# Performance work log

Hardware: AMD Instinct MI355X
Metric: run time of the kernel (lower is better)

## Reference

```python
import jax, jax.numpy as jnp
import numpy as np

D_MODEL = 1024
NUM_HEADS = 16
D_K = D_MODEL // NUM_HEADS


def setup_inputs() -> dict:
    key = jax.random.key(0)
    k1, k2, k3, k4 = jax.random.split(key, 4)
    x = jax.random.normal(k1, (2, 2048, D_MODEL), dtype=jnp.float32)
    # qkv_proj: Linear(d_model, 3*d_model, bias=False); stored as [in, out] for x @ W
    W_qkv = jax.random.normal(k2, (D_MODEL, 3 * D_MODEL), dtype=jnp.float32) * (1.0 / np.sqrt(D_MODEL))
    W_out = jax.random.normal(k3, (D_MODEL, D_MODEL), dtype=jnp.float32) * (1.0 / np.sqrt(D_MODEL))
    b_out = jax.random.normal(k4, (D_MODEL,), dtype=jnp.float32) * 0.01
    return {"x": x, "W_qkv": W_qkv, "W_out": W_out, "b_out": b_out}


def reference(x, W_qkv, W_out, b_out):
    B, N, C = x.shape
    scale = 1.0 / np.sqrt(D_K)
    qkv = (x @ W_qkv).reshape(B, N, 3, NUM_HEADS, D_K)
    qkv = jnp.transpose(qkv, (2, 0, 3, 1, 4))  # [3, B, H, N, d_k]
    q, k, v = qkv[0], qkv[1], qkv[2]
    scores = jnp.einsum("bhqd,bhkd->bhqk", q, k) * scale  # [B,H,N,N]
    attn = jax.nn.softmax(scores, axis=-1)
    out = jnp.einsum("bhqk,bhkd->bhqd", attn, v)  # [B,H,N,d_k]
    out = jnp.transpose(out, (0, 2, 1, 3)).reshape(B, N, C)
    return out @ W_out + b_out
```

## Files before the change

### kernel.cpp

```cpp
#include <hip/hip_runtime.h>
#include <cstdint>

typedef __bf16 bf16_t;
typedef __bf16 bf16x4 __attribute__((ext_vector_type(4)));
typedef __bf16 bf16x8 __attribute__((ext_vector_type(8)));
typedef float  f32x4  __attribute__((ext_vector_type(4)));
typedef uint32_t u32x4 __attribute__((ext_vector_type(4)));

#define MFMA16(a,b,c) __builtin_amdgcn_mfma_f32_16x16x32_bf16((a),(b),(c),0,0,0)
#define BAR()    __builtin_amdgcn_s_barrier()
#define VMW(n)   asm volatile("s_waitcnt vmcnt(" #n ")" ::: "memory")

__device__ __forceinline__ void gload_lds16(const bf16_t* g, bf16_t* l) {
  __builtin_amdgcn_global_load_lds(
      (const __attribute__((address_space(1))) unsigned int*)g,
      (__attribute__((address_space(3))) unsigned int*)l,
      16, 0, 0);
}

__device__ __forceinline__ uint32_t cvt_pk_bf16(float lo, float hi) {
  uint32_t r;
  asm("v_cvt_pk_bf16_f32 %0, %1, %2" : "=v"(r) : "v"(lo), "v"(hi));
  return r;
}

__global__ void k_conv_x(const float* __restrict__ x, bf16_t* __restrict__ xb) {
  int i = blockIdx.x * blockDim.x + threadIdx.x;
  const float4* p = reinterpret_cast<const float4*>(x) + (size_t)i * 2;
  float4 a = p[0], b = p[1];
  bf16x8 v;
  v[0]=(bf16_t)a.x; v[1]=(bf16_t)a.y; v[2]=(bf16_t)a.z; v[3]=(bf16_t)a.w;
  v[4]=(bf16_t)b.x; v[5]=(bf16_t)b.y; v[6]=(bf16_t)b.z; v[7]=(bf16_t)b.w;
  *reinterpret_cast<bf16x8*>(xb + (size_t)i * 8) = v;
}

__global__ void k_transpose_w2(const float* __restrict__ Wq, bf16_t* __restrict__ WqT,
                               const float* __restrict__ Wo, bf16_t* __restrict__ WoT) {
  __shared__ float tile[32][33];
  int bx = blockIdx.x;
  const float* W; bf16_t* WT; int N, n0;
  if (bx < 96) { W = Wq; WT = WqT; N = 3072; n0 = bx * 32; }
  else         { W = Wo; WT = WoT; N = 1024; n0 = (bx - 96) * 32; }
  int k0 = blockIdx.y * 32;
  int c = threadIdx.x & 31, r8 = threadIdx.x >> 5;
#pragma unroll
  for (int rr = 0; rr < 4; rr++) {
    int r = r8 + rr * 8;
    tile[r][c] = W[(size_t)(k0 + r) * N + n0 + c];
  }
  __syncthreads();
#pragma unroll
  for (int rr = 0; rr < 4; rr++) {
    int r = r8 + rr * 8;
    WT[(size_t)(n0 + r) * 1024 + k0 + c] = (bf16_t)tile[c][r];
  }
}

template<int EPI, int MT, int NT>
__global__ __launch_bounds__(256, 2) void k_gemm(
    const bf16_t* __restrict__ A, const bf16_t* __restrict__ BT, int Klen,
    bf16_t* __restrict__ Qo, bf16_t* __restrict__ Ko, bf16_t* __restrict__ Vt,
    const float* __restrict__ bias, float* __restrict__ Out, int Nout) {
  constexpr int WM = MT / 2;
  constexpr int MF = WM / 16;
  constexpr int WN = NT / 2;
  constexpr int NF = WN / 16;
  __shared__ bf16_t As[2][MT * 32];
  __shared__ bf16_t Bs[2][NT * 32];
  int tid = threadIdx.x, lane = tid & 63, wid = tid >> 6;
  int row0 = blockIdx.x * MT, col0 = blockIdx.y * NT;
  int wr = wid >> 1, wc = wid & 1;
  int g = lane >> 4, li = lane & 15;

  f32x4 acc[MF][NF] = {};

  auto stage = [&](int buf, int kt) {
    int k0 = kt * 32;
#pragma unroll
    for (int j = 0; j < MT / 64; j++) {
      int q = tid + 256 * j;
      int r = q >> 2, part = q & 3;
      gload_lds16(A + (size_t)(row0 + r) * Klen + k0 + part * 8,
                  &As[buf][q * 8]);
    }
#pragma unroll
    for (int j = 0; j < NT / 64; j++) {
      int q = tid + 256 * j;
      int r = q >> 2, part = q & 3;
      gload_lds16(BT + (size_t)(col0 + r) * Klen + k0 + part * 8,
                  &Bs[buf][q * 8]);
    }
  };

  int nk = Klen >> 5;
  stage(0, 0);
  for (int kt = 0; kt < nk; kt++) {
    __syncthreads();
    if (kt + 1 < nk) stage((kt + 1) & 1, kt + 1);
    int buf = kt & 1;
    int kl = g * 8;
    bf16x8 a[MF], b[NF];
#pragma unroll
    for (int m = 0; m < MF; m++)
      a[m] = *reinterpret_cast<const bf16x8*>(&As[buf][(wr * WM + m * 16 + li) * 32 + kl]);
#pragma unroll
    for (int n = 0; n < NF; n++)
      b[n] = *reinterpret_cast<const bf16x8*>(&Bs[buf][(wc * WN + n * 16 + li) * 32 + kl]);
#pragma unroll
    for (int m = 0; m < MF; m++)
#pragma unroll
      for (int n = 0; n < NF; n++)
        acc[m][n] = MFMA16(a[m], b[n], acc[m][n]);
  }

#pragma unroll
  for (int m = 0; m < MF; m++) {
    int rg = row0 + wr * WM + m * 16 + g * 4;
    int b2 = rg >> 11, nn0 = rg & 2047;
#pragma unroll
    for (int n = 0; n < NF; n++) {
      int cg = col0 + wc * WN + n * 16 + li;
      if constexpr (EPI == 0) {
        int t = cg >> 10, h = (cg >> 6) & 15, dk = cg & 63;
        int head = (b2 << 4) + h;
        if (t == 2) {
          bf16x4 pv;
#pragma unroll
          for (int ii = 0; ii < 4; ii++) pv[ii] = (bf16_t)acc[m][n][ii];
          *reinterpret_cast<bf16x4*>(
              &Vt[(size_t)head * 131072 + (size_t)dk * 2048 + nn0]) = pv;
        } else {
#pragma unroll
          for (int ii = 0; ii < 4; ii++) {
            float v = acc[m][n][ii];
            size_t idx = ((size_t)head * 2048 + nn0 + ii) * 64 + dk;
            if (t == 0) Qo[idx] = (bf16_t)(v * 0.18033688011112042f);
            else        Ko[idx] = (bf16_t)v;
          }
        }
      } else {
#pragma unroll
        for (int ii = 0; ii < 4; ii++)
          Out[(size_t)(rg + ii) * Nout + cg] = acc[m][n][ii] + bias[cg];
      }
    }
  }
}

__global__ __launch_bounds__(256, 2) void k_flash(
    const bf16_t* __restrict__ Q, const bf16_t* __restrict__ K,
    const bf16_t* __restrict__ VT, bf16_t* __restrict__ O) {
  __shared__ bf16_t Ks[3][64 * 64];
  __shared__ bf16_t Vs[3][64 * 64];

  int bi = (blockIdx.x & 7) * 64 + (blockIdx.x >> 3);
  int head = bi >> 4, qt = bi & 15;
  int tid = threadIdx.x, lane = tid & 63, wid = tid >> 6;
  int g = lane >> 4, li = lane & 15;

  const bf16_t* Qh = Q + (size_t)head * 131072 + (size_t)qt * 128 * 64;
  const bf16_t* Kh = K + (size_t)head * 131072;
  const bf16_t* Vh = VT + (size_t)head * 131072;

  bf16x8 qf[2][2];
#pragma unroll
  for (int rg = 0; rg < 2; rg++) {
    const bf16_t* qrow = Qh + (size_t)(wid * 32 + rg * 16 + li) * 64;
    qf[rg][0] = *reinterpret_cast<const bf16x8*>(qrow + g * 8);
    qf[rg][1] = *reinterpret_cast<const bf16x8*>(qrow + 32 + g * 8);
  }

  u32x4 onesw;
  onesw[0] = 0x3F803F80u; onesw[1] = 0x3F803F80u;
  onesw[2] = 0x3F803F80u; onesw[3] = 0x3F803F80u;
  bf16x8 ones = __builtin_bit_cast(bf16x8, onesw);

  f32x4 zero4 = {};
  f32x4 o[2][4] = {};
  f32x4 osum[2] = {};

  auto stage = [&](int buf, int t) {
    int kv0 = t * 64;
#pragma unroll
    for (int j = 0; j < 2; j++) {
      int q = tid + 256 * j;
      int key = q >> 3, part = q & 7;
      int sw = (key & 7) ^ (((key >> 3) & 3) << 1);
      gload_lds16(Kh + (size_t)(kv0 + key) * 64 + ((part ^ sw) * 8),
                  &Ks[buf][(tid + j * 256) * 8]);
    }
#pragma unroll
    for (int j = 0; j < 2; j++) {
      int q = tid + 256 * j;
      int dv = q >> 3, part = q & 7;
      gload_lds16(Vh + (size_t)dv * 2048 + kv0 + ((part ^ (dv & 7)) * 8),
                  &Vs[buf][(tid + j * 256) * 8]);
    }
  };

  stage(0, 0);
  stage(1, 1);
  for (int t = 0; t < 32; t++) {
    if (t < 31) { VMW(4); } else { VMW(0); }
    BAR();
    __builtin_amdgcn_sched_barrier(0);
    if (t + 2 < 32) stage((t + 2) % 3, t + 2);
    int buf = t % 3;
    char* KsB = (char*)&Ks[buf][0];
    char* VsB = (char*)&Vs[buf][0];

    bf16x8 ka[2][4];
#pragma unroll
    for (int kd = 0; kd < 2; kd++)
#pragma unroll
      for (int nf = 0; nf < 4; nf++) {
        int key = ((li >> 2) << 3) | ((nf & 1) << 2) | (li & 3) | ((nf >> 1) << 5);
        int sw = (key & 7) ^ (((key >> 3) & 3) << 1);
        ka[kd][nf] = *reinterpret_cast<const bf16x8*>(
            KsB + key * 128 + (((kd * 4 + g) ^ sw) << 4));
      }

    f32x4 s[2][4];
    __builtin_amdgcn_s_setprio(1);
#pragma unroll
    for (int nf = 0; nf < 4; nf++) {
      s[0][nf] = MFMA16(ka[0][nf], qf[0][0], zero4);
      s[1][nf] = MFMA16(ka[0][nf], qf[1][0], zero4);
    }
#pragma unroll
    for (int nf = 0; nf < 4; nf++) {
      s[0][nf] = MFMA16(ka[1][nf], qf[0][1], s[0][nf]);
      s[1][nf] = MFMA16(ka[1][nf], qf[1][1], s[1][nf]);
    }
    __builtin_amdgcn_s_setprio(0);

    bf16x8 pa[2][2];
#pragma unroll
    for (int rg = 0; rg < 2; rg++) {
#pragma unroll
      for (int nf = 0; nf < 4; nf++)
#pragma unroll
        for (int i = 0; i < 4; i++)
          s[rg][nf][i] = __builtin_amdgcn_exp2f(s[rg][nf][i]);
      u32x4 w0, w1;
      w0[0] = cvt_pk_bf16(s[rg][0][0], s[rg][0][1]);
      w0[1] = cvt_pk_bf16(s[rg][0][2], s[rg][0][3]);
      w0[2] = cvt_pk_bf16(s[rg][1][0], s[rg][1][1]);
      w0[3] = cvt_pk_bf16(s[rg][1][2], s[rg][1][3]);
      w1[0] = cvt_pk_bf16(s[rg][2][0], s[rg][2][1]);
      w1[1] = cvt_pk_bf16(s[rg][2][2], s[rg][2][3]);
      w1[2] = cvt_pk_bf16(s[rg][3][0], s[rg][3][1]);
      w1[3] = cvt_pk_bf16(s[rg][3][2], s[rg][3][3]);
      pa[rg][0] = __builtin_bit_cast(bf16x8, w0);
      pa[rg][1] = __builtin_bit_cast(bf16x8, w1);
    }

    __builtin_amdgcn_s_setprio(1);
    osum[0] = MFMA16(pa[0][0], ones, osum[0]);
    osum[0] = MFMA16(pa[0][1], ones, osum[0]);
    osum[1] = MFMA16(pa[1][0], ones, osum[1]);
    osum[1] = MFMA16(pa[1][1], ones, osum[1]);
#pragma unroll
    for (int nfv = 0; nfv < 4; nfv++) {
      int dv = nfv * 16 + li;
      bf16x8 b0 = *reinterpret_cast<const bf16x8*>(
          VsB + dv * 128 + ((g * 16) ^ ((dv & 7) << 4)));
      bf16x8 b1 = *reinterpret_cast<const bf16x8*>(
          VsB + dv * 128 + ((64 + g * 16) ^ ((dv & 7) << 4)));
      o[0][nfv] = MFMA16(pa[0][0], b0, o[0][nfv]);
      o[0][nfv] = MFMA16(pa[0][1], b1, o[0][nfv]);
      o[1][nfv] = MFMA16(pa[1][0], b0, o[1][nfv]);
      o[1][nfv] = MFMA16(pa[1][1], b1, o[1][nfv]);
    }
    __builtin_amdgcn_s_setprio(0);
  }

  int b2 = head >> 4, h = head & 15;
#pragma unroll
  for (int rg = 0; rg < 2; rg++) {
#pragma unroll
    for (int i = 0; i < 4; i++) {
      float inv = 1.f / osum[rg][i];
      int n = qt * 128 + wid * 32 + rg * 16 + g * 4 + i;
      size_t base = ((size_t)b2 * 2048 + n) * 1024 + h * 64;
#pragma unroll
      for (int nfv = 0; nfv < 4; nfv++)
        O[base + nfv * 16 + li] = (bf16_t)(o[rg][nfv][i] * inv);
    }
  }
}

extern "C" void kernel_launch(void* const* d_in, const int* in_sizes, int n_in,
                              void* d_out, int out_size, void* d_ws, size_t ws_size,
                              hipStream_t stream) {
  const float* x    = (const float*)d_in[0];
  const float* Wqkv = (const float*)d_in[1];
  const float* Wout = (const float*)d_in[2];
  const float* bout = (const float*)d_in[3];
  float* out = (float*)d_out;

  char* ws = (char*)d_ws;
  bf16_t* xb    = (bf16_t*)(ws);
  bf16_t* wqkvT = (bf16_t*)(ws + ((size_t)8  << 20));
  bf16_t* woutT = (bf16_t*)(ws + ((size_t)14 << 20));
  bf16_t* qw    = (bf16_t*)(ws + ((size_t)16 << 20));
  bf16_t* kw    = (bf16_t*)(ws + ((size_t)24 << 20));
  bf16_t* vtw   = (bf16_t*)(ws + ((size_t)40 << 20));
  bf16_t* ow    = (bf16_t*)(ws + ((size_t)48 << 20));

  k_conv_x<<<2048, 256, 0, stream>>>(x, xb);
  k_transpose_w2<<<dim3(128, 32), 256, 0, stream>>>(Wqkv, wqkvT, Wout, woutT);
  k_gemm<0, 128, 192><<<dim3(32, 16), 256, 0, stream>>>(
      xb, wqkvT, 1024, qw, kw, vtw, nullptr, nullptr, 0);
  k_flash<<<512, 256, 0, stream>>>(qw, kw, vtw, ow);
  k_gemm<1, 64, 128><<<dim3(64, 8), 256, 0, stream>>>(
      ow, woutT, 1024, nullptr, nullptr, nullptr, bout, out, 1024);
}
```

Measured before the change: 107.3 us.

## Split flash waves over query and key halves, merge prep kernels

The attention kernel now arranges its four waves as two query groups by two key halves. Each wave computes 64 query rows against 32 keys per tile, so each K and V fragment read from LDS feeds four MFMAs instead of two. Partial outputs and row sums from the two key halves are combined through LDS in the epilogue, which adds a barrier and more accumulator registers. The x conversion and weight transpose kernels are also merged into a single launch to save a kernel launch.

```diff
diff --git a/kernel.cpp b/kernel.cpp
--- a/kernel.cpp
+++ b/kernel.cpp
@@ -24,24 +24,26 @@
   return r;
 }
 
-__global__ void k_conv_x(const float* __restrict__ x, bf16_t* __restrict__ xb) {
-  int i = blockIdx.x * blockDim.x + threadIdx.x;
-  const float4* p = reinterpret_cast<const float4*>(x) + (size_t)i * 2;
-  float4 a = p[0], b = p[1];
-  bf16x8 v;
-  v[0]=(bf16_t)a.x; v[1]=(bf16_t)a.y; v[2]=(bf16_t)a.z; v[3]=(bf16_t)a.w;
-  v[4]=(bf16_t)b.x; v[5]=(bf16_t)b.y; v[6]=(bf16_t)b.z; v[7]=(bf16_t)b.w;
-  *reinterpret_cast<bf16x8*>(xb + (size_t)i * 8) = v;
-}
-
-__global__ void k_transpose_w2(const float* __restrict__ Wq, bf16_t* __restrict__ WqT,
-                               const float* __restrict__ Wo, bf16_t* __restrict__ WoT) {
+__global__ void k_prep(const float* __restrict__ x, bf16_t* __restrict__ xb,
+                       const float* __restrict__ Wq, bf16_t* __restrict__ WqT,
+                       const float* __restrict__ Wo, bf16_t* __restrict__ WoT) {
   __shared__ float tile[32][33];
-  int bx = blockIdx.x;
+  int bid = blockIdx.x;
+  if (bid < 2048) {
+    int i = bid * blockDim.x + threadIdx.x;
+    const float4* p = reinterpret_cast<const float4*>(x) + (size_t)i * 2;
+    float4 a = p[0], b = p[1];
+    bf16x8 v;
+    v[0]=(bf16_t)a.x; v[1]=(bf16_t)a.y; v[2]=(bf16_t)a.z; v[3]=(bf16_t)a.w;
+    v[4]=(bf16_t)b.x; v[5]=(bf16_t)b.y; v[6]=(bf16_t)b.z; v[7]=(bf16_t)b.w;
+    *reinterpret_cast<bf16x8*>(xb + (size_t)i * 8) = v;
+    return;
+  }
+  int t = bid - 2048;
+  int bx = t & 127, k0 = (t >> 7) * 32;
   const float* W; bf16_t* WT; int N, n0;
   if (bx < 96) { W = Wq; WT = WqT; N = 3072; n0 = bx * 32; }
   else         { W = Wo; WT = WoT; N = 1024; n0 = (bx - 96) * 32; }
-  int k0 = blockIdx.y * 32;
   int c = threadIdx.x & 31, r8 = threadIdx.x >> 5;
 #pragma unroll
   for (int rr = 0; rr < 4; rr++) {
@@ -156,18 +158,19 @@
   int bi = (blockIdx.x & 7) * 64 + (blockIdx.x >> 3);
   int head = bi >> 4, qt = bi & 15;
   int tid = threadIdx.x, lane = tid & 63, wid = tid >> 6;
+  int qg = wid >> 1, kg = wid & 1;
   int g = lane >> 4, li = lane & 15;
 
   const bf16_t* Qh = Q + (size_t)head * 131072 + (size_t)qt * 128 * 64;
   const bf16_t* Kh = K + (size_t)head * 131072;
   const bf16_t* Vh = VT + (size_t)head * 131072;
 
-  bf16x8 qf[2][2];
-#pragma unroll
-  for (int rg = 0; rg < 2; rg++) {
-    const bf16_t* qrow = Qh + (size_t)(wid * 32 + rg * 16 + li) * 64;
-    qf[rg][0] = *reinterpret_cast<const bf16x8*>(qrow + g * 8);
-    qf[rg][1] = *reinterpret_cast<const bf16x8*>(qrow + 32 + g * 8);
+  bf16x8 qf[4][2];
+#pragma unroll
+  for (int nq = 0; nq < 4; nq++) {
+    const bf16_t* qrow = Qh + (size_t)(qg * 64 + nq * 16 + li) * 64;
+    qf[nq][0] = *reinterpret_cast<const bf16x8*>(qrow + g * 8);
+    qf[nq][1] = *reinterpret_cast<const bf16x8*>(qrow + 32 + g * 8);
   }
 
   u32x4 onesw;
@@ -176,8 +179,8 @@
   bf16x8 ones = __builtin_bit_cast(bf16x8, onesw);
 
   f32x4 zero4 = {};
-  f32x4 o[2][4] = {};
-  f32x4 osum[2] = {};
+  f32x4 o[4][4] = {};
+  f32x4 osum[4] = {};
 
   auto stage = [&](int buf, int t) {
     int kv0 = t * 64;
@@ -209,83 +212,98 @@
     char* KsB = (char*)&Ks[buf][0];
     char* VsB = (char*)&Vs[buf][0];
 
-    bf16x8 ka[2][4];
+    bf16x8 ka[2][2];
 #pragma unroll
     for (int kd = 0; kd < 2; kd++)
 #pragma unroll
-      for (int nf = 0; nf < 4; nf++) {
-        int key = ((li >> 2) << 3) | ((nf & 1) << 2) | (li & 3) | ((nf >> 1) << 5);
+      for (int c = 0; c < 2; c++) {
+        int key = kg * 32 + ((li >> 2) << 3) + c * 4 + (li & 3);
         int sw = (key & 7) ^ (((key >> 3) & 3) << 1);
-        ka[kd][nf] = *reinterpret_cast<const bf16x8*>(
+        ka[kd][c] = *reinterpret_cast<const bf16x8*>(
             KsB + key * 128 + (((kd * 4 + g) ^ sw) << 4));
       }
 
     f32x4 s[2][4];
     __builtin_amdgcn_s_setprio(1);
 #pragma unroll
-    for (int nf = 0; nf < 4; nf++) {
-      s[0][nf] = MFMA16(ka[0][nf], qf[0][0], zero4);
-      s[1][nf] = MFMA16(ka[0][nf], qf[1][0], zero4);
-    }
-#pragma unroll
-    for (int nf = 0; nf < 4; nf++) {
-      s[0][nf] = MFMA16(ka[1][nf], qf[0][1], s[0][nf]);
-      s[1][nf] = MFMA16(ka[1][nf], qf[1][1], s[1][nf]);
-    }
+    for (int c = 0; c < 2; c++)
+#pragma unroll
+      for (int nq = 0; nq < 4; nq++)
+        s[c][nq] = MFMA16(ka[0][c], qf[nq][0], zero4);
+#pragma unroll
+    for (int c = 0; c < 2; c++)
+#pragma unroll
+      for (int nq = 0; nq < 4; nq++)
+        s[c][nq] = MFMA16(ka[1][c], qf[nq][1], s[c][nq]);
     __builtin_amdgcn_s_setprio(0);
 
-    bf16x8 pa[2][2];
-#pragma unroll
-    for (int rg = 0; rg < 2; rg++) {
-#pragma unroll
-      for (int nf = 0; nf < 4; nf++)
+    bf16x8 pa[4];
+#pragma unroll
+    for (int c = 0; c < 2; c++)
+#pragma unroll
+      for (int nq = 0; nq < 4; nq++)
 #pragma unroll
         for (int i = 0; i < 4; i++)
-          s[rg][nf][i] = __builtin_amdgcn_exp2f(s[rg][nf][i]);
-      u32x4 w0, w1;
-      w0[0] = cvt_pk_bf16(s[rg][0][0], s[rg][0][1]);
-      w0[1] = cvt_pk_bf16(s[rg][0][2], s[rg][0][3]);
-      w0[2] = cvt_pk_bf16(s[rg][1][0], s[rg][1][1]);
-      w0[3] = cvt_pk_bf16(s[rg][1][2], s[rg][1][3]);
-      w1[0] = cvt_pk_bf16(s[rg][2][0], s[rg][2][1]);
-      w1[1] = cvt_pk_bf16(s[rg][2][2], s[rg][2][3]);
-      w1[2] = cvt_pk_bf16(s[rg][3][0], s[rg][3][1]);
-      w1[3] = cvt_pk_bf16(s[rg][3][2], s[rg][3][3]);
-      pa[rg][0] = __builtin_bit_cast(bf16x8, w0);
-      pa[rg][1] = __builtin_bit_cast(bf16x8, w1);
+          s[c][nq][i] = __builtin_amdgcn_exp2f(s[c][nq][i]);
+#pragma unroll
+    for (int nq = 0; nq < 4; nq++) {
+      u32x4 w;
+      w[0] = cvt_pk_bf16(s[0][nq][0], s[0][nq][1]);
+      w[1] = cvt_pk_bf16(s[0][nq][2], s[0][nq][3]);
+      w[2] = cvt_pk_bf16(s[1][nq][0], s[1][nq][1]);
+      w[3] = cvt_pk_bf16(s[1][nq][2], s[1][nq][3]);
+      pa[nq] = __builtin_bit_cast(bf16x8, w);
     }
 
     __builtin_amdgcn_s_setprio(1);
-    osum[0] = MFMA16(pa[0][0], ones, osum[0]);
-    osum[0] = MFMA16(pa[0][1], ones, osum[0]);
-    osum[1] = MFMA16(pa[1][0], ones, osum[1]);
-    osum[1] = MFMA16(pa[1][1], ones, osum[1]);
-#pragma unroll
-    for (int nfv = 0; nfv < 4; nfv++) {
-      int dv = nfv * 16 + li;
-      bf16x8 b0 = *reinterpret_cast<const bf16x8*>(
-          VsB + dv * 128 + ((g * 16) ^ ((dv & 7) << 4)));
-      bf16x8 b1 = *reinterpret_cast<const bf16x8*>(
-          VsB + dv * 128 + ((64 + g * 16) ^ ((dv & 7) << 4)));
-      o[0][nfv] = MFMA16(pa[0][0], b0, o[0][nfv]);
-      o[0][nfv] = MFMA16(pa[0][1], b1, o[0][nfv]);
-      o[1][nfv] = MFMA16(pa[1][0], b0, o[1][nfv]);
-      o[1][nfv] = MFMA16(pa[1][1], b1, o[1][nfv]);
+#pragma unroll
+    for (int nq = 0; nq < 4; nq++)
+      osum[nq] = MFMA16(pa[nq], ones, osum[nq]);
+#pragma unroll
+    for (int ndv = 0; ndv < 4; ndv++) {
+      int dv = ndv * 16 + li;
+      bf16x8 b = *reinterpret_cast<const bf16x8*>(
+          VsB + dv * 128 + ((kg * 64 + g * 16) ^ ((dv & 7) << 4)));
+#pragma unroll
+      for (int nq = 0; nq < 4; nq++)
+        o[nq][ndv] = MFMA16(pa[nq], b, o[nq][ndv]);
     }
     __builtin_amdgcn_s_setprio(0);
   }
 
-  int b2 = head >> 4, h = head & 15;
-#pragma unroll
-  for (int rg = 0; rg < 2; rg++) {
-#pragma unroll
-    for (int i = 0; i < 4; i++) {
-      float inv = 1.f / osum[rg][i];
-      int n = qt * 128 + wid * 32 + rg * 16 + g * 4 + i;
-      size_t base = ((size_t)b2 * 2048 + n) * 1024 + h * 64;
-#pragma unroll
-      for (int nfv = 0; nfv < 4; nfv++)
-        O[base + nfv * 16 + li] = (bf16_t)(o[rg][nfv][i] * inv);
+  __syncthreads();
+  float* dump = (float*)&Ks[0][0] + qg * 5120;
+  if (kg == 1) {
+#pragma unroll
+    for (int nq = 0; nq < 4; nq++)
+#pragma unroll
+      for (int ndv = 0; ndv < 4; ndv++)
+#pragma unroll
+        for (int i = 0; i < 4; i++)
+          dump[(((nq * 4 + ndv) * 4) + i) * 64 + lane] = o[nq][ndv][i];
+#pragma unroll
+    for (int nq = 0; nq < 4; nq++)
+#pragma unroll
+      for (int i = 0; i < 4; i++)
+        dump[4096 + (nq * 4 + i) * 64 + lane] = osum[nq][i];
+  }
+  __syncthreads();
+  if (kg == 0) {
+    int b2 = head >> 4, h = head & 15;
+#pragma unroll
+    for (int nq = 0; nq < 4; nq++) {
+#pragma unroll
+      for (int i = 0; i < 4; i++) {
+        float ltot = osum[nq][i] + dump[4096 + (nq * 4 + i) * 64 + lane];
+        float inv = 1.f / ltot;
+        int n = qt * 128 + qg * 64 + nq * 16 + g * 4 + i;
+        size_t base = ((size_t)b2 * 2048 + n) * 1024 + h * 64;
+#pragma unroll
+        for (int ndv = 0; ndv < 4; ndv++) {
+          float tot = o[nq][ndv][i] + dump[(((nq * 4 + ndv) * 4) + i) * 64 + lane];
+          O[base + ndv * 16 + li] = (bf16_t)(tot * inv);
+        }
+      }
     }
   }
 }
@@ -308,8 +326,7 @@
   bf16_t* vtw   = (bf16_t*)(ws + ((size_t)40 << 20));
   bf16_t* ow    = (bf16_t*)(ws + ((size_t)48 << 20));
 
-  k_conv_x<<<2048, 256, 0, stream>>>(x, xb);
-  k_transpose_w2<<<dim3(128, 32), 256, 0, stream>>>(Wqkv, wqkvT, Wout, woutT);
+  k_prep<<<2048 + 4096, 256, 0, stream>>>(x, xb, Wqkv, wqkvT, Wout, woutT);
   k_gemm<0, 128, 192><<<dim3(32, 16), 256, 0, stream>>>(
       xb, wqkvT, 1024, qw, kw, vtw, nullptr, nullptr, 0);
   k_flash<<<512, 256, 0, stream>>>(qw, kw, vtw, ow);
```

Result: no change. 105.6 us (-1.6%).
